# Kernel optimization log

Measured on AMD Instinct MI355X. Metric: run time of the kernel, lower is better.

## Reference

```python
import jax, jax.numpy as jnp
import numpy as np

POOL_OUT = 100  # AdaptiveAvgPool1d target length
SCALE = np.sqrt(256.0).astype(np.float32)


def setup_inputs() -> dict:
    key = jax.random.key(0)
    ks = jax.random.split(key, 5)
    B, F, T = 16, 512, 4000
    x = jax.random.normal(ks[0], (B, F, T), dtype=jnp.float32)
    Wk = jax.random.normal(ks[1], (256, 100), dtype=jnp.float32) * 0.05
    bk = jax.random.normal(ks[2], (256,), dtype=jnp.float32) * 0.05
    Wq = jax.random.normal(ks[3], (256, 100), dtype=jnp.float32) * 0.05
    bq = jax.random.normal(ks[4], (256,), dtype=jnp.float32) * 0.05
    return {"x": x, "Wk": Wk, "bk": bk, "Wq": Wq, "bq": bq}


def reference(x, Wk, bk, Wq, bq):
    B, F, T = x.shape
    # AdaptiveAvgPool1d(100): T divisible by 100 -> mean over contiguous windows
    pooled = x.reshape(B, F, POOL_OUT, T // POOL_OUT).mean(axis=-1)  # [B,F,100]
    key = pooled @ Wk.T + bk    # [B,F,256]
    query = pooled @ Wq.T + bq  # [B,F,256]
    att = jax.nn.softmax(jnp.einsum('bfd,bgd->bfg', key, query) / SCALE, axis=2)  # [B,F,F]
    # the per-step loop sum+concat is exactly att @ x
    cat = jnp.einsum('bfg,bgt->bft', att, x)  # [B,F,T]
    fw = cat.mean(axis=2, keepdims=True)      # [B,F,1]
    mi = fw.min(axis=1, keepdims=True)
    ma = fw.max(axis=1, keepdims=True)
    fw_n = (fw - mi) / (ma - mi) + 1e-6
    return x * fw_n
```

## Files before the change

### kernel.cpp

```cpp
#include <hip/hip_runtime.h>
#include <hip/hip_bf16.h>
#include <math.h>

#define B_ 16
#define F_ 512
#define T_ 4000
#define D_ 100
#define E_ 256
#define ROWS (B_*F_)

typedef __attribute__((ext_vector_type(8))) short short8;
typedef __attribute__((ext_vector_type(4))) float f32x4;

__global__ __launch_bounds__(256) void k_pool(const float* __restrict__ x,
                                              float* __restrict__ pooled,
                                              float* __restrict__ xmean) {
    __shared__ float buf[T_];
    __shared__ float part[4];
    const int row = blockIdx.x;
    const int tid = threadIdx.x;
    const float4* xr = (const float4*)(x + (size_t)row * T_);
    float4* b4 = (float4*)buf;
    for (int i = tid; i < T_/4; i += 256) b4[i] = xr[i];
    __syncthreads();
    float s = 0.f;
    if (tid < 200) {
        const float4* p = (const float4*)(buf + 20 * tid);
        float4 a0 = p[0], a1 = p[1], a2 = p[2], a3 = p[3], a4 = p[4];
        s  = a0.x + a0.y + a0.z + a0.w;
        s += a1.x + a1.y + a1.z + a1.w;
        s += a2.x + a2.y + a2.z + a2.w;
        s += a3.x + a3.y + a3.z + a3.w;
        s += a4.x + a4.y + a4.z + a4.w;
    }
    float other = __shfl_xor(s, 1);
    if (tid < 200 && (tid & 1) == 0)
        pooled[(size_t)row * D_ + (tid >> 1)] = (s + other) * (1.0f/40.0f);
    float tot = s;
    #pragma unroll
    for (int off = 32; off; off >>= 1) tot += __shfl_xor(tot, off);
    if ((tid & 63) == 0) part[tid >> 6] = tot;
    __syncthreads();
    if (tid == 0)
        xmean[row] = (part[0] + part[1] + part[2] + part[3]) * (1.0f/(float)T_);
}

__global__ __launch_bounds__(256) void k_kq(const float* __restrict__ pooled,
                                            const float* __restrict__ Wk,
                                            const float* __restrict__ bk,
                                            const float* __restrict__ Wq,
                                            const float* __restrict__ bq,
                                            short* __restrict__ Khi,
                                            short* __restrict__ Klo,
                                            short* __restrict__ Qhi,
                                            short* __restrict__ Qlo) {
    __shared__ float As[D_][65];
    __shared__ float Bs[D_][65];
    const int m0 = blockIdx.x * 64;
    const int n0 = blockIdx.y * 64;
    const int tid = threadIdx.x;

    const float* Ab = pooled + (size_t)m0 * D_;
    for (int i = tid; i < 64 * D_; i += 256) {
        int r = i / D_, k = i - r * D_;
        As[k][r] = Ab[i];
    }
    const float* Wb = (n0 < E_) ? (Wk + (size_t)n0 * D_) : (Wq + (size_t)(n0 - E_) * D_);
    for (int i = tid; i < 64 * D_; i += 256) {
        int r = i / D_, k = i - r * D_;
        Bs[k][r] = Wb[i];
    }
    __syncthreads();

    const int tm = (tid >> 4) * 4;
    const int tn = (tid & 15) * 4;
    float acc[4][4] = {};
    for (int k = 0; k < D_; ++k) {
        float a[4], b[4];
        #pragma unroll
        for (int i = 0; i < 4; ++i) a[i] = As[k][tm + i];
        #pragma unroll
        for (int j = 0; j < 4; ++j) b[j] = Bs[k][tn + j];
        #pragma unroll
        for (int i = 0; i < 4; ++i)
            #pragma unroll
            for (int j = 0; j < 4; ++j)
                acc[i][j] = fmaf(a[i], b[j], acc[i][j]);
    }
    const bool is_key = (n0 < E_);
    short* __restrict__ Phi = is_key ? Khi : Qhi;
    short* __restrict__ Plo = is_key ? Klo : Qlo;
    #pragma unroll
    for (int i = 0; i < 4; ++i)
        #pragma unroll
        for (int jj = 0; jj < 4; ++jj) {
            int n = n0 + tn + jj;
            float bias = is_key ? bk[n] : bq[n - E_];
            float val = acc[i][jj] + bias;
            int mg = m0 + tm + i;
            int b = mg >> 9, f = mg & 511;
            int e = is_key ? n : (n - E_);
            size_t idx = (((size_t)b * 32 + (f >> 4)) * 32 + (e >> 3)) * 128
                       + (size_t)(f & 15) * 8 + (e & 7);
            __hip_bfloat16 h = __float2bfloat16(val);
            float hf = __bfloat162float(h);
            __hip_bfloat16 l = __float2bfloat16(val - hf);
            Phi[idx] = *(short*)&h;
            Plo[idx] = *(short*)&l;
        }
}

__global__ __launch_bounds__(256) void k_scores(const short* __restrict__ Khi,
                                                const short* __restrict__ Klo,
                                                const short* __restrict__ Qhi,
                                                const short* __restrict__ Qlo,
                                                float* __restrict__ S) {
    const int b    = blockIdx.z;
    const int f0   = blockIdx.x * 64;
    const int g0   = blockIdx.y * 64;
    const int w    = threadIdx.x >> 6;
    const int lane = threadIdx.x & 63;
    const int gt   = (g0 >> 4) + w;
    const size_t qbase = (((size_t)b * 32 + gt) << 12) + (size_t)lane * 8;
    const size_t abase = (((size_t)b * 32 + (f0 >> 4)) << 12) + (size_t)lane * 8;
    f32x4 acc[4] = {};
    #pragma unroll
    for (int s = 0; s < 8; ++s) {
        short8 bh = *(const short8*)(Qhi + qbase + s * 512);
        short8 bl = *(const short8*)(Qlo + qbase + s * 512);
        #pragma unroll
        for (int mt = 0; mt < 4; ++mt) {
            short8 ah = *(const short8*)(Khi + abase + mt * 4096 + s * 512);
            short8 al = *(const short8*)(Klo + abase + mt * 4096 + s * 512);
            acc[mt] = __builtin_amdgcn_mfma_f32_16x16x32_bf16(ah, bh, acc[mt], 0, 0, 0);
            acc[mt] = __builtin_amdgcn_mfma_f32_16x16x32_bf16(ah, bl, acc[mt], 0, 0, 0);
            acc[mt] = __builtin_amdgcn_mfma_f32_16x16x32_bf16(al, bh, acc[mt], 0, 0, 0);
        }
    }
    const int col = lane & 15, quad = lane >> 4;
    float* Sb = S + ((size_t)b * F_ + f0) * 512 + g0 + w * 16 + col;
    #pragma unroll
    for (int mt = 0; mt < 4; ++mt)
        #pragma unroll
        for (int r = 0; r < 4; ++r)
            Sb[(size_t)(mt * 16 + quad * 4 + r) * 512] = acc[mt][r] * (1.0f/16.0f);
}

__global__ __launch_bounds__(256) void k_softmax_fw(const float* __restrict__ S,
                                                    const float* __restrict__ xmean,
                                                    float* __restrict__ fw) {
    const int row  = blockIdx.x * 4 + (threadIdx.x >> 6);
    const int lane = threadIdx.x & 63;
    const int b    = row >> 9;
    const float4* Sr = (const float4*)(S + (size_t)row * 512);
    const float4* xm = (const float4*)(xmean + ((size_t)b << 9));
    float4 v0 = Sr[lane * 2], v1 = Sr[lane * 2 + 1];
    float m = fmaxf(fmaxf(fmaxf(v0.x, v0.y), fmaxf(v0.z, v0.w)),
                    fmaxf(fmaxf(v1.x, v1.y), fmaxf(v1.z, v1.w)));
    #pragma unroll
    for (int off = 32; off; off >>= 1) m = fmaxf(m, __shfl_xor(m, off));
    float4 x0 = xm[lane * 2], x1 = xm[lane * 2 + 1];
    float sum = 0.f, dot = 0.f, p;
    p = expf(v0.x - m); sum += p; dot += p * x0.x;
    p = expf(v0.y - m); sum += p; dot += p * x0.y;
    p = expf(v0.z - m); sum += p; dot += p * x0.z;
    p = expf(v0.w - m); sum += p; dot += p * x0.w;
    p = expf(v1.x - m); sum += p; dot += p * x1.x;
    p = expf(v1.y - m); sum += p; dot += p * x1.y;
    p = expf(v1.z - m); sum += p; dot += p * x1.z;
    p = expf(v1.w - m); sum += p; dot += p * x1.w;
    #pragma unroll
    for (int off = 32; off; off >>= 1) {
        sum += __shfl_xor(sum, off);
        dot += __shfl_xor(dot, off);
    }
    if (lane == 0) fw[row] = dot / sum;
}

__global__ __launch_bounds__(512) void k_norm(const float* __restrict__ fw,
                                              float* __restrict__ fwn) {
    __shared__ float rmin[512];
    __shared__ float rmax[512];
    const int b = blockIdx.x, tid = threadIdx.x;
    float v = fw[b * F_ + tid];
    rmin[tid] = v; rmax[tid] = v;
    __syncthreads();
    for (int s = 256; s > 0; s >>= 1) {
        if (tid < s) {
            rmin[tid] = fminf(rmin[tid], rmin[tid + s]);
            rmax[tid] = fmaxf(rmax[tid], rmax[tid + s]);
        }
        __syncthreads();
    }
    float mi = rmin[0], ma = rmax[0];
    fwn[b * F_ + tid] = (v - mi) / (ma - mi) + 1e-6f;
}

__global__ __launch_bounds__(256) void k_scale(const float* __restrict__ x,
                                               const float* __restrict__ fwn,
                                               float* __restrict__ out) {
    const int row = blockIdx.x;
    const float s = fwn[row];
    const float4* xr = (const float4*)(x + (size_t)row * T_);
    float4* orow = (float4*)(out + (size_t)row * T_);
    for (int i = threadIdx.x; i < T_/4; i += 256) {
        float4 v = xr[i];
        v.x *= s; v.y *= s; v.z *= s; v.w *= s;
        orow[i] = v;
    }
}

extern "C" void kernel_launch(void* const* d_in, const int* in_sizes, int n_in,
                              void* d_out, int out_size, void* d_ws, size_t ws_size,
                              hipStream_t stream) {
    const float* x  = (const float*)d_in[0];
    const float* Wk = (const float*)d_in[1];
    const float* bk = (const float*)d_in[2];
    const float* Wq = (const float*)d_in[3];
    const float* bq = (const float*)d_in[4];
    float* out = (float*)d_out;

    float* ws     = (float*)d_ws;
    float* pooled = ws;
    float* xmean  = pooled + (size_t)ROWS * D_;
    float* S      = xmean + ROWS;
    float* fw     = S + (size_t)B_ * F_ * F_;
    float* fwn    = fw + ROWS;
    short* Khi    = (short*)(fwn + ROWS);
    short* Klo    = Khi + (size_t)B_ * 32 * 4096;
    short* Qhi    = Klo + (size_t)B_ * 32 * 4096;
    short* Qlo    = Qhi + (size_t)B_ * 32 * 4096;

    k_pool<<<ROWS, 256, 0, stream>>>(x, pooled, xmean);
    k_kq<<<dim3(ROWS/64, 512/64), 256, 0, stream>>>(pooled, Wk, bk, Wq, bq,
                                                    Khi, Klo, Qhi, Qlo);
    k_scores<<<dim3(F_/64, F_/64, B_), 256, 0, stream>>>(Khi, Klo, Qhi, Qlo, S);
    k_softmax_fw<<<ROWS/4, 256, 0, stream>>>(S, xmean, fw);
    k_norm<<<B_, 512, 0, stream>>>(fw, fwn);
    k_scale<<<ROWS, 256, 0, stream>>>(x, fwn, out);
}
```

Baseline: 317.1 us.

## Fuse score matmul with online softmax-weighted mean and fold normalization into scale

Replaces the separate score, softmax and min/max normalization kernels with one attention kernel. Each block computes a 16-row strip of scores with MFMA, applies the softmax, and takes the dot product with the row means, combining per-wave partials with an online max rescale. This avoids writing and re-reading the 16 MB score matrix. The per-batch min/max reduction moves into the final scale kernel, where each block recomputes it redundantly. The cost is fewer blocks (512) in the fused kernel, each doing more serial work.

```diff
diff --git a/kernel.cpp b/kernel.cpp
--- a/kernel.cpp
+++ b/kernel.cpp
@@ -110,100 +110,114 @@
         }
 }
 
-__global__ __launch_bounds__(256) void k_scores(const short* __restrict__ Khi,
-                                                const short* __restrict__ Klo,
-                                                const short* __restrict__ Qhi,
-                                                const short* __restrict__ Qlo,
-                                                float* __restrict__ S) {
-    const int b    = blockIdx.z;
-    const int f0   = blockIdx.x * 64;
-    const int g0   = blockIdx.y * 64;
-    const int w    = threadIdx.x >> 6;
-    const int lane = threadIdx.x & 63;
-    const int gt   = (g0 >> 4) + w;
-    const size_t qbase = (((size_t)b * 32 + gt) << 12) + (size_t)lane * 8;
-    const size_t abase = (((size_t)b * 32 + (f0 >> 4)) << 12) + (size_t)lane * 8;
-    f32x4 acc[4] = {};
+__global__ __launch_bounds__(256) void k_att(const short* __restrict__ Khi,
+                                             const short* __restrict__ Klo,
+                                             const short* __restrict__ Qhi,
+                                             const short* __restrict__ Qlo,
+                                             const float* __restrict__ xmean,
+                                             float* __restrict__ fw) {
+    const int ft  = blockIdx.x;
+    const int b   = blockIdx.y;
+    const int tid = threadIdx.x;
+    const int w    = tid >> 6;
+    const int lane = tid & 63;
+    const int col  = lane & 15;
+    const int quad = lane >> 4;
+
+    __shared__ float xm[512];
+    __shared__ float cm[4][16], cs[4][16], cd[4][16];
+    xm[tid]       = xmean[((size_t)b << 9) + tid];
+    xm[tid + 256] = xmean[((size_t)b << 9) + 256 + tid];
+
+    const size_t kbase = ((((size_t)b * 32 + ft) << 12)) + (size_t)lane * 8;
+    short8 kh[8], kl[8];
     #pragma unroll
     for (int s = 0; s < 8; ++s) {
-        short8 bh = *(const short8*)(Qhi + qbase + s * 512);
-        short8 bl = *(const short8*)(Qlo + qbase + s * 512);
-        #pragma unroll
-        for (int mt = 0; mt < 4; ++mt) {
-            short8 ah = *(const short8*)(Khi + abase + mt * 4096 + s * 512);
-            short8 al = *(const short8*)(Klo + abase + mt * 4096 + s * 512);
-            acc[mt] = __builtin_amdgcn_mfma_f32_16x16x32_bf16(ah, bh, acc[mt], 0, 0, 0);
-            acc[mt] = __builtin_amdgcn_mfma_f32_16x16x32_bf16(ah, bl, acc[mt], 0, 0, 0);
-            acc[mt] = __builtin_amdgcn_mfma_f32_16x16x32_bf16(al, bh, acc[mt], 0, 0, 0);
-        }
-    }
-    const int col = lane & 15, quad = lane >> 4;
-    float* Sb = S + ((size_t)b * F_ + f0) * 512 + g0 + w * 16 + col;
-    #pragma unroll
-    for (int mt = 0; mt < 4; ++mt)
-        #pragma unroll
-        for (int r = 0; r < 4; ++r)
-            Sb[(size_t)(mt * 16 + quad * 4 + r) * 512] = acc[mt][r] * (1.0f/16.0f);
-}
-
-__global__ __launch_bounds__(256) void k_softmax_fw(const float* __restrict__ S,
-                                                    const float* __restrict__ xmean,
-                                                    float* __restrict__ fw) {
-    const int row  = blockIdx.x * 4 + (threadIdx.x >> 6);
-    const int lane = threadIdx.x & 63;
-    const int b    = row >> 9;
-    const float4* Sr = (const float4*)(S + (size_t)row * 512);
-    const float4* xm = (const float4*)(xmean + ((size_t)b << 9));
-    float4 v0 = Sr[lane * 2], v1 = Sr[lane * 2 + 1];
-    float m = fmaxf(fmaxf(fmaxf(v0.x, v0.y), fmaxf(v0.z, v0.w)),
-                    fmaxf(fmaxf(v1.x, v1.y), fmaxf(v1.z, v1.w)));
-    #pragma unroll
-    for (int off = 32; off; off >>= 1) m = fmaxf(m, __shfl_xor(m, off));
-    float4 x0 = xm[lane * 2], x1 = xm[lane * 2 + 1];
-    float sum = 0.f, dot = 0.f, p;
-    p = expf(v0.x - m); sum += p; dot += p * x0.x;
-    p = expf(v0.y - m); sum += p; dot += p * x0.y;
-    p = expf(v0.z - m); sum += p; dot += p * x0.z;
-    p = expf(v0.w - m); sum += p; dot += p * x0.w;
-    p = expf(v1.x - m); sum += p; dot += p * x1.x;
-    p = expf(v1.y - m); sum += p; dot += p * x1.y;
-    p = expf(v1.z - m); sum += p; dot += p * x1.z;
-    p = expf(v1.w - m); sum += p; dot += p * x1.w;
-    #pragma unroll
-    for (int off = 32; off; off >>= 1) {
-        sum += __shfl_xor(sum, off);
-        dot += __shfl_xor(dot, off);
-    }
-    if (lane == 0) fw[row] = dot / sum;
-}
-
-__global__ __launch_bounds__(512) void k_norm(const float* __restrict__ fw,
-                                              float* __restrict__ fwn) {
-    __shared__ float rmin[512];
-    __shared__ float rmax[512];
-    const int b = blockIdx.x, tid = threadIdx.x;
-    float v = fw[b * F_ + tid];
-    rmin[tid] = v; rmax[tid] = v;
-    __syncthreads();
-    for (int s = 256; s > 0; s >>= 1) {
-        if (tid < s) {
-            rmin[tid] = fminf(rmin[tid], rmin[tid + s]);
-            rmax[tid] = fmaxf(rmax[tid], rmax[tid + s]);
-        }
-        __syncthreads();
-    }
-    float mi = rmin[0], ma = rmax[0];
-    fwn[b * F_ + tid] = (v - mi) / (ma - mi) + 1e-6f;
+        kh[s] = *(const short8*)(Khi + kbase + s * 512);
+        kl[s] = *(const short8*)(Klo + kbase + s * 512);
+    }
+
+    f32x4 acc[8] = {};
+    #pragma unroll 2
+    for (int j = 0; j < 8; ++j) {
+        const size_t qb = ((((size_t)b * 32 + (w * 8 + j)) << 12)) + (size_t)lane * 8;
+        #pragma unroll
+        for (int s = 0; s < 8; ++s) {
+            short8 qh = *(const short8*)(Qhi + qb + s * 512);
+            short8 ql = *(const short8*)(Qlo + qb + s * 512);
+            acc[j] = __builtin_amdgcn_mfma_f32_16x16x32_bf16(kh[s], qh, acc[j], 0, 0, 0);
+            acc[j] = __builtin_amdgcn_mfma_f32_16x16x32_bf16(kh[s], ql, acc[j], 0, 0, 0);
+            acc[j] = __builtin_amdgcn_mfma_f32_16x16x32_bf16(kl[s], qh, acc[j], 0, 0, 0);
+        }
+    }
+    __syncthreads();
+
+    #pragma unroll
+    for (int r = 0; r < 4; ++r) {
+        float v[8];
+        #pragma unroll
+        for (int j = 0; j < 8; ++j) v[j] = acc[j][r] * (1.0f / 16.0f);
+        float mx = v[0];
+        #pragma unroll
+        for (int j = 1; j < 8; ++j) mx = fmaxf(mx, v[j]);
+        #pragma unroll
+        for (int off = 8; off; off >>= 1) mx = fmaxf(mx, __shfl_xor(mx, off));
+        float se = 0.f, de = 0.f;
+        #pragma unroll
+        for (int j = 0; j < 8; ++j) {
+            float p = expf(v[j] - mx);
+            se += p;
+            de += p * xm[(w * 8 + j) * 16 + col];
+        }
+        #pragma unroll
+        for (int off = 8; off; off >>= 1) {
+            se += __shfl_xor(se, off);
+            de += __shfl_xor(de, off);
+        }
+        if (col == 0) {
+            cm[w][quad * 4 + r] = mx;
+            cs[w][quad * 4 + r] = se;
+            cd[w][quad * 4 + r] = de;
+        }
+    }
+    __syncthreads();
+    if (tid < 16) {
+        float M = fmaxf(fmaxf(cm[0][tid], cm[1][tid]), fmaxf(cm[2][tid], cm[3][tid]));
+        float S = 0.f, D = 0.f;
+        #pragma unroll
+        for (int ww = 0; ww < 4; ++ww) {
+            float e = expf(cm[ww][tid] - M);
+            S += cs[ww][tid] * e;
+            D += cd[ww][tid] * e;
+        }
+        fw[((size_t)b << 9) + ft * 16 + tid] = D / S;
+    }
 }
 
 __global__ __launch_bounds__(256) void k_scale(const float* __restrict__ x,
-                                               const float* __restrict__ fwn,
+                                               const float* __restrict__ fw,
                                                float* __restrict__ out) {
     const int row = blockIdx.x;
-    const float s = fwn[row];
+    const int b   = row >> 9;
+    const int tid = threadIdx.x;
+    const float* fb = fw + ((size_t)b << 9);
+    float v0 = fb[tid], v1 = fb[tid + 256];
+    float mi = fminf(v0, v1), ma = fmaxf(v0, v1);
+    #pragma unroll
+    for (int off = 32; off; off >>= 1) {
+        mi = fminf(mi, __shfl_xor(mi, off));
+        ma = fmaxf(ma, __shfl_xor(ma, off));
+    }
+    __shared__ float smi[4], sma[4];
+    if ((tid & 63) == 0) { smi[tid >> 6] = mi; sma[tid >> 6] = ma; }
+    __syncthreads();
+    mi = fminf(fminf(smi[0], smi[1]), fminf(smi[2], smi[3]));
+    ma = fmaxf(fmaxf(sma[0], sma[1]), fmaxf(sma[2], sma[3]));
+    const float s = (fw[row] - mi) / (ma - mi) + 1e-6f;
+
     const float4* xr = (const float4*)(x + (size_t)row * T_);
     float4* orow = (float4*)(out + (size_t)row * T_);
-    for (int i = threadIdx.x; i < T_/4; i += 256) {
+    for (int i = tid; i < T_/4; i += 256) {
         float4 v = xr[i];
         v.x *= s; v.y *= s; v.z *= s; v.w *= s;
         orow[i] = v;
@@ -223,10 +237,8 @@
     float* ws     = (float*)d_ws;
     float* pooled = ws;
     float* xmean  = pooled + (size_t)ROWS * D_;
-    float* S      = xmean + ROWS;
-    float* fw     = S + (size_t)B_ * F_ * F_;
-    float* fwn    = fw + ROWS;
-    short* Khi    = (short*)(fwn + ROWS);
+    float* fw     = xmean + ROWS;
+    short* Khi    = (short*)(fw + ROWS);
     short* Klo    = Khi + (size_t)B_ * 32 * 4096;
     short* Qhi    = Klo + (size_t)B_ * 32 * 4096;
     short* Qlo    = Qhi + (size_t)B_ * 32 * 4096;
@@ -234,8 +246,6 @@
     k_pool<<<ROWS, 256, 0, stream>>>(x, pooled, xmean);
     k_kq<<<dim3(ROWS/64, 512/64), 256, 0, stream>>>(pooled, Wk, bk, Wq, bq,
                                                     Khi, Klo, Qhi, Qlo);
-    k_scores<<<dim3(F_/64, F_/64, B_), 256, 0, stream>>>(Khi, Klo, Qhi, Qlo, S);
-    k_softmax_fw<<<ROWS/4, 256, 0, stream>>>(S, xmean, fw);
-    k_norm<<<B_, 512, 0, stream>>>(fw, fwn);
-    k_scale<<<ROWS, 256, 0, stream>>>(x, fwn, out);
-}
+    k_att<<<dim3(F_/16, B_), 256, 0, stream>>>(Khi, Klo, Qhi, Qlo, xmean, fw);
+    k_scale<<<ROWS, 256, 0, stream>>>(x, fw, out);
+}
```

After: 322.5 us. About the same (+1.7%).
